# Performance work log

Measured on AMD Instinct MI355X. Metric: run time of the kernel, lower is better.

Reference implementation:

```python
import jax, jax.numpy as jnp
import numpy as np

EMBED = 1024
HEADS = 16
DH = EMBED // HEADS
B, S = 2, 2048


def setup_inputs() -> dict:
    key = jax.random.key(0)
    ks = jax.random.split(key, 12)
    inp = {
        "k": jax.random.normal(ks[0], (B, S, EMBED), jnp.float32),
        "q": jax.random.normal(ks[1], (B, S, EMBED), jnp.float32),
        "v": jax.random.normal(ks[2], (B, S, EMBED), jnp.float32),
        "mask": jax.random.randint(ks[3], (B, 1, S, S), 0, 2, jnp.int32),
        # per-head projections (shared across heads, as in the torch module)
        "Wk": jax.random.normal(ks[4], (DH, DH), jnp.float32) / np.sqrt(DH),
        "bk": jnp.zeros((DH,), jnp.float32),
        "Wq": jax.random.normal(ks[5], (DH, DH), jnp.float32) / np.sqrt(DH),
        "bq": jnp.zeros((DH,), jnp.float32),
        "Wv": jax.random.normal(ks[6], (DH, DH), jnp.float32) / np.sqrt(DH),
        "bv": jnp.zeros((DH,), jnp.float32),
        "Wo": jax.random.normal(ks[7], (EMBED, EMBED), jnp.float32) / np.sqrt(EMBED),
        "bo": jnp.zeros((EMBED,), jnp.float32),
    }
    return inp


def reference(k, q, v, mask, Wk, bk, Wq, bq, Wv, bv, Wo, bo):
    b, s, _ = k.shape
    sq = q.shape[1]
    # [B,S,H,dh]
    kh = k.reshape(b, s, HEADS, DH)
    qh = q.reshape(b, sq, HEADS, DH)
    vh = v.reshape(b, s, HEADS, DH)
    # per-head linear (weight shared across heads): x @ W.T + b
    kh = kh @ Wk.T + bk
    qh = qh @ Wq.T + bq
    vh = vh @ Wv.T + bv
    # scores [B,H,Sq,Sk]
    product = jnp.einsum("bqhd,bkhd->bhqk", qh, kh)
    # masked_fill BEFORE scaling, as in the original
    product = jnp.where(mask == 0, jnp.float32(-1e20), product)
    product = product / np.sqrt(DH)
    scores = jax.nn.softmax(product, axis=-1)
    ctx = jnp.einsum("bhqk,bkhd->bqhd", scores, vh).reshape(b, sq, EMBED)
    return ctx @ Wo.T + bo
```

## Files before the change

### kernel.cpp

```cpp
#include <hip/hip_runtime.h>
#include <hip/hip_bf16.h>
#include <math.h>

#define EMBED 1024
#define HEADS 16
#define DH    64
#define BATCH 2
#define SEQ   2048

typedef __attribute__((ext_vector_type(8))) short bf16x8;
typedef __attribute__((ext_vector_type(4))) short bf16x4;
typedef __attribute__((ext_vector_type(4))) float f32x4;
typedef unsigned long long u64;
typedef __attribute__((ext_vector_type(2))) unsigned long long u64x2;

#define QSCALE 0.1803368801111244f

static __device__ __forceinline__ unsigned short f2bf(float x) {
    unsigned u = __builtin_bit_cast(unsigned, x);
    return (unsigned short)((u + 0x7fffu + ((u >> 16) & 1u)) >> 16);
}
static __device__ __forceinline__ unsigned pk2bf(float a, float b) {
    union { __hip_bfloat162 h2; unsigned u; } c;
    c.h2 = __float22bfloat162_rn(make_float2(a, b));
    return c.u;
}
static __device__ __forceinline__ float fexp2(float x) {
#if __has_builtin(__builtin_amdgcn_exp2f)
    return __builtin_amdgcn_exp2f(x);
#else
    float r; asm("v_exp_f32 %0, %1" : "=v"(r) : "v"(x)); return r;
#endif
}
static __device__ __forceinline__ void gl_lds16(const void* g, void* l) {
    __builtin_amdgcn_global_load_lds(
        (const __attribute__((address_space(1))) void*)g,
        (__attribute__((address_space(3))) void*)l, 16, 0, 0);
}
static __device__ __forceinline__ bf16x8 cvt8(const float* p) {
    float4 a = ((const float4*)p)[0];
    float4 b = ((const float4*)p)[1];
    union { unsigned u[4]; bf16x8 v; } c;
    c.u[0] = pk2bf(a.x, a.y); c.u[1] = pk2bf(a.z, a.w);
    c.u[2] = pk2bf(b.x, b.y); c.u[3] = pk2bf(b.z, b.w);
    return c.v;
}

__global__ __launch_bounds__(256) void proj_mfma(
    const float* __restrict__ q, const float* __restrict__ k, const float* __restrict__ v,
    const float* __restrict__ Wq, const float* __restrict__ bq,
    const float* __restrict__ Wk, const float* __restrict__ bk,
    const float* __restrict__ Wv, const float* __restrict__ bv,
    unsigned short* __restrict__ qh, unsigned short* __restrict__ kh,
    unsigned short* __restrict__ vt,
    const int* __restrict__ mask, u64* __restrict__ bits,
    const float* __restrict__ Wo, unsigned short* __restrict__ Wob)
{
    const int blk   = blockIdx.x;
    const int which = blockIdx.y;
    const int t     = threadIdx.x;

    if (which == 3) {
        if (blk < 512) {
            const int idx = blk * 256 + t;
            const int4* src = (const int4*)(mask + (size_t)idx * 64);
            u64 wb = 0;
#pragma unroll
            for (int u = 0; u < 16; ++u) {
                int4 m = src[u];
                u64 nib = (m.x != 0 ? 1ull : 0) | (m.y != 0 ? 2ull : 0) |
                          (m.z != 0 ? 4ull : 0) | (m.w != 0 ? 8ull : 0);
                wb |= nib << (u * 4);
            }
            bits[idx] = wb;
        } else {
            const int i = ((blk - 512) * 256 + t) * 8;
            float4 a = ((const float4*)(Wo + i))[0];
            float4 b = ((const float4*)(Wo + i))[1];
            unsigned o32[4] = {pk2bf(a.x, a.y), pk2bf(a.z, a.w),
                               pk2bf(b.x, b.y), pk2bf(b.z, b.w)};
            *(uint4*)(Wob + i) = *(uint4*)o32;
        }
        return;
    }

    const float* x; const float* W; const float* bias;
    if (which == 0)      { x = q; W = Wq; bias = bq; }
    else if (which == 1) { x = k; W = Wk; bias = bk; }
    else                 { x = v; W = Wv; bias = bv; }

    __shared__ unsigned short Ws[64 * 72];

    const int w    = t >> 6;
    const int lane = t & 63;
    const int l15  = lane & 15;
    const int quad = lane >> 4;

    const int sr = t >> 2, sp = t & 3;
    {
        const float* wsrc = W + (size_t)sr * 64 + sp * 16;
        unsigned o32[8];
#pragma unroll
        for (int u4 = 0; u4 < 4; ++u4) {
            float4 a = ((const float4*)wsrc)[u4];
            o32[u4 * 2 + 0] = pk2bf(a.x, a.y);
            o32[u4 * 2 + 1] = pk2bf(a.z, a.w);
        }
        *(uint4*)&Ws[sr * 72 + sp * 16]     = *(uint4*)&o32[0];
        *(uint4*)&Ws[sr * 72 + sp * 16 + 8] = *(uint4*)&o32[4];
    }

    if (which == 2) {
        const int bh = blk >> 5;
        const int st = blk & 31;
        const int b  = bh >> 4, h = bh & 15;
        const int s  = st * 64 + w * 16 + l15;

        const float* xrow = x + ((size_t)(b * SEQ + s)) * EMBED + h * DH;
        const bf16x8 bx0 = cvt8(xrow + quad * 8);
        const bf16x8 bx1 = cvt8(xrow + 32 + quad * 8);

        __syncthreads();

#pragma unroll
        for (int nt = 0; nt < 4; ++nt) {
            bf16x8 aw0 = *(const bf16x8*)&Ws[(nt * 16 + l15) * 72 + quad * 8];
            bf16x8 aw1 = *(const bf16x8*)&Ws[(nt * 16 + l15) * 72 + 32 + quad * 8];
            f32x4 a = {0, 0, 0, 0};
            a = __builtin_amdgcn_mfma_f32_16x16x32_bf16(aw0, bx0, a, 0, 0, 0);
            a = __builtin_amdgcn_mfma_f32_16x16x32_bf16(aw1, bx1, a, 0, 0, 0);
#pragma unroll
            for (int r = 0; r < 4; ++r) {
                const int d = nt * 16 + quad * 4 + r;
                vt[((size_t)bh * DH + d) * SEQ + s] = f2bf(a[r] + bias[d]);
            }
        }
        return;
    }

    const float oscale = (which == 0) ? QSCALE : 1.0f;
    unsigned short* out = (which == 0) ? qh : kh;

    const float* xrow = x + ((size_t)blk * 64 + w * 16 + l15) * 64;
    const bf16x8 bx0 = cvt8(xrow + quad * 8);
    const bf16x8 bx1 = cvt8(xrow + 32 + quad * 8);

    __syncthreads();

    const int bs = blk * 4 + w;
    const int b = bs >> 11, s = bs & 2047;
    unsigned short* obase = out + (((size_t)b * HEADS + l15) * SEQ + s) * DH + quad * 4;

#pragma unroll
    for (int nt = 0; nt < 4; ++nt) {
        bf16x8 aw0 = *(const bf16x8*)&Ws[(nt * 16 + l15) * 72 + quad * 8];
        bf16x8 aw1 = *(const bf16x8*)&Ws[(nt * 16 + l15) * 72 + 32 + quad * 8];
        f32x4 a = {0, 0, 0, 0};
        a = __builtin_amdgcn_mfma_f32_16x16x32_bf16(aw0, bx0, a, 0, 0, 0);
        a = __builtin_amdgcn_mfma_f32_16x16x32_bf16(aw1, bx1, a, 0, 0, 0);
        const int d0 = nt * 16 + quad * 4;
        const float4 bb = *(const float4*)&bias[d0];
        unsigned o2[2] = {pk2bf((a[0] + bb.x) * oscale, (a[1] + bb.y) * oscale),
                          pk2bf((a[2] + bb.z) * oscale, (a[3] + bb.w) * oscale)};
        *(uint2*)(obase + nt * 16) = *(uint2*)o2;
    }
}

__global__ __launch_bounds__(256, 2) void attn_kernel(
    const unsigned short* __restrict__ qh, const unsigned short* __restrict__ kh,
    const unsigned short* __restrict__ vt, const u64* __restrict__ mbits,
    unsigned short* __restrict__ ctx)
{
    const int bid = blockIdx.x;
    const int bh  = bid & 31;
    const int q0  = (bid >> 5) * 128;
    const int b   = bh >> 4;

    __shared__ unsigned char smem[65536];

    const int t    = threadIdx.x;
    const int w    = t >> 6;
    const int lane = t & 63;
    const int l15  = lane & 15;
    const int quad = lane >> 4;

    const int srow   = lane >> 3;
    const int schunk = (lane & 7) ^ srow;

    bf16x8 qf[2][2];
#pragma unroll
    for (int g = 0; g < 2; ++g) {
        const unsigned short* qb =
            qh + ((size_t)bh * SEQ + q0 + w * 32 + g * 16 + l15) * DH + quad * 8;
        qf[g][0] = *(const bf16x8*)qb;
        qf[g][1] = *(const bf16x8*)(qb + 32);
    }

    f32x4 O[2][4];
#pragma unroll
    for (int g = 0; g < 2; ++g)
#pragma unroll
        for (int dt = 0; dt < 4; ++dt) O[g][dt] = f32x4{0, 0, 0, 0};
    f32x4 Osum[2] = {f32x4{0, 0, 0, 0}, f32x4{0, 0, 0, 0}};
    const bf16x4 ones = {(short)0x3F80, (short)0x3F80, (short)0x3F80, (short)0x3F80};

    const unsigned short* kbase = kh + (size_t)bh * SEQ * DH
                                  + (size_t)srow * DH + schunk * 8;
    const unsigned short* vbase = vt + (size_t)bh * DH * SEQ
                                  + (size_t)srow * SEQ + schunk * 8;
    const u64* mrow0 = mbits + ((size_t)b * SEQ + q0 + w * 32 + l15) * (SEQ / 64);
    const u64* mrow1 = mrow0 + 16 * (SEQ / 64);

    auto stage = [&](int kp, unsigned char* buf) {
#pragma unroll
        for (int j = 0; j < 8; ++j) {
            const int idx = w * 8 + j;
            if (idx < 16) {
                const int u = idx >> 3, i = idx & 7;
                gl_lds16(kbase + ((size_t)kp * 128 + u * 64 + i * 8) * DH,
                         buf + u * 8192 + i * 1024);
            } else {
                const int u = (idx - 16) >> 3, i = (idx - 16) & 7;
                gl_lds16(vbase + kp * 128 + u * 64 + (size_t)i * 8 * SEQ,
                         buf + 16384 + u * 8192 + i * 1024);
            }
        }
    };

    stage(0, smem);
    u64 pm00 = mrow0[0], pm01 = mrow0[1], pm10 = mrow1[0], pm11 = mrow1[1];
    __syncthreads();

    for (int it = 0; it < 16; ++it) {
        u64x2 nA, nB;
        if (it < 15) {
            nA = *(const u64x2*)&mrow0[2 * it + 2];
            nB = *(const u64x2*)&mrow1[2 * it + 2];
            stage(it + 1, smem + ((it + 1) & 1) * 32768);
            asm volatile("s_waitcnt vmcnt(10)" ::: "memory");
        } else {
            asm volatile("s_waitcnt vmcnt(0)" ::: "memory");
        }
        __builtin_amdgcn_s_barrier();
        __builtin_amdgcn_sched_barrier(0);

        const unsigned char* buf = smem + (it & 1) * 32768;

        __builtin_amdgcn_s_setprio(1);
#pragma unroll
        for (int u = 0; u < 2; ++u) {
            const unsigned short* KtH = (const unsigned short*)(buf + u * 8192);
            const unsigned short* VtH = (const unsigned short*)(buf + 16384 + u * 8192);
            const u64 mq0 = (u ? pm01 : pm00) >> (quad * 4);
            const u64 mq1 = (u ? pm11 : pm10) >> (quad * 4);

            bf16x4 p[2][4];
            const int rx = l15 & 7;
#pragma unroll
            for (int st = 0; st < 4; ++st) {
                const int r = st * 16 + l15;
                bf16x8 kf0 = *(const bf16x8*)&KtH[r * 64 + ((quad ^ rx)) * 8];
                bf16x8 kf1 = *(const bf16x8*)&KtH[r * 64 + ((quad ^ rx) ^ 4) * 8];
#pragma unroll
                for (int g = 0; g < 2; ++g) {
                    f32x4 sa = {0, 0, 0, 0};
                    sa = __builtin_amdgcn_mfma_f32_16x16x32_bf16(kf0, qf[g][0], sa, 0, 0, 0);
                    sa = __builtin_amdgcn_mfma_f32_16x16x32_bf16(kf1, qf[g][1], sa, 0, 0, 0);
                    const unsigned nib =
                        (unsigned)((g ? mq1 : mq0) >> (st * 16)) & 0xFu;
                    float p0 = (nib & 1u) ? fexp2(sa[0]) : 0.f;
                    float p1 = (nib & 2u) ? fexp2(sa[1]) : 0.f;
                    float p2 = (nib & 4u) ? fexp2(sa[2]) : 0.f;
                    float p3 = (nib & 8u) ? fexp2(sa[3]) : 0.f;
                    union { unsigned u2[2]; bf16x4 v; } pu;
                    pu.u2[0] = pk2bf(p0, p1);
                    pu.u2[1] = pk2bf(p2, p3);
                    p[g][st] = pu.v;
                    Osum[g] = __builtin_amdgcn_mfma_f32_16x16x16bf16_1k(
                        p[g][st], ones, Osum[g], 0, 0, 0);
                }
            }

#pragma unroll
            for (int dt = 0; dt < 4; ++dt) {
                const int d = dt * 16 + l15;
                const int dx = l15 & 7;
#pragma unroll
                for (int st = 0; st < 4; ++st) {
                    const int ch = (st * 2 + (quad >> 1)) ^ dx;
                    bf16x4 vb = *(const bf16x4*)&VtH[d * 64 + ch * 8 + (quad & 1) * 4];
                    O[0][dt] = __builtin_amdgcn_mfma_f32_16x16x16bf16_1k(
                        p[0][st], vb, O[0][dt], 0, 0, 0);
                    O[1][dt] = __builtin_amdgcn_mfma_f32_16x16x16bf16_1k(
                        p[1][st], vb, O[1][dt], 0, 0, 0);
                }
            }
        }
        __builtin_amdgcn_s_setprio(0);
        __builtin_amdgcn_sched_barrier(0);
        __builtin_amdgcn_s_barrier();

        if (it < 15) { pm00 = nA[0]; pm01 = nA[1]; pm10 = nB[0]; pm11 = nB[1]; }
    }

#pragma unroll
    for (int g = 0; g < 2; ++g) {
        float inv[4];
#pragma unroll
        for (int r = 0; r < 4; ++r) inv[r] = 1.0f / Osum[g][r];
#pragma unroll
        for (int r = 0; r < 4; ++r) {
            const int row = q0 + w * 32 + g * 16 + quad * 4 + r;
            unsigned short* dst = ctx + ((size_t)bh * SEQ + row) * DH + l15;
#pragma unroll
            for (int dt = 0; dt < 4; ++dt)
                dst[dt * 16] = f2bf(O[g][dt][r] * inv[r]);
        }
    }
}

__global__ __launch_bounds__(256, 3) void outproj_mfma(
    const unsigned short* __restrict__ ctx, const unsigned short* __restrict__ Wob,
    const float* __restrict__ bo, float* __restrict__ out)
{
    const int n0 = blockIdx.x * 64;
    const int m0 = blockIdx.y * 128;
    const int b  = m0 / SEQ;
    const int s0 = m0 % SEQ;

    __shared__ unsigned char smem[49152];

    const int t    = threadIdx.x;
    const int w    = t >> 6;
    const int lane = t & 63;
    const int l15  = lane & 15;
    const int quad = lane >> 4;
    const int srow   = lane >> 3;
    const int schunk = (lane & 7) ^ srow;

    const unsigned short* abase = ctx + ((size_t)b * HEADS * SEQ + s0 + srow) * DH + schunk * 8;
    const unsigned short* wbase = Wob + (size_t)(n0 + srow) * EMBED + schunk * 8;

    f32x4 acc[8];
#pragma unroll
    for (int mt = 0; mt < 8; ++mt) acc[mt] = f32x4{0, 0, 0, 0};

    auto stage = [&](int kt, unsigned char* buf) {
#pragma unroll
        for (int j = 0; j < 6; ++j) {
            const int idx = w * 6 + j;
            if (idx < 16)
                gl_lds16(abase + (size_t)kt * SEQ * DH + (size_t)idx * 8 * DH,
                         buf + idx * 1024);
            else
                gl_lds16(wbase + (size_t)(idx - 16) * 8 * EMBED + kt * 64,
                         buf + 16384 + (idx - 16) * 1024);
        }
    };

    stage(0, smem);
    __syncthreads();

    for (int kt = 0; kt < 16; ++kt) {
        if (kt < 15) stage(kt + 1, smem + ((kt + 1) & 1) * 24576);

        const unsigned char* buf = smem + (kt & 1) * 24576;
        const unsigned short* At = (const unsigned short*)buf;
        const unsigned short* Wt = (const unsigned short*)(buf + 16384);
        const int rx = l15 & 7;
        const int c0 = ((quad ^ rx)) * 8;

        __builtin_amdgcn_s_setprio(1);
        bf16x8 bf0 = *(const bf16x8*)&Wt[(w * 16 + l15) * 64 + c0];
        bf16x8 bf1 = *(const bf16x8*)&Wt[(w * 16 + l15) * 64 + (c0 ^ 32)];
#pragma unroll
        for (int mt = 0; mt < 8; ++mt) {
            bf16x8 af0 = *(const bf16x8*)&At[(mt * 16 + l15) * 64 + c0];
            bf16x8 af1 = *(const bf16x8*)&At[(mt * 16 + l15) * 64 + (c0 ^ 32)];
            acc[mt] = __builtin_amdgcn_mfma_f32_16x16x32_bf16(af0, bf0, acc[mt], 0, 0, 0);
            acc[mt] = __builtin_amdgcn_mfma_f32_16x16x32_bf16(af1, bf1, acc[mt], 0, 0, 0);
        }
        __builtin_amdgcn_s_setprio(0);
        __syncthreads();
    }

    const float bv = bo[n0 + w * 16 + l15];
#pragma unroll
    for (int mt = 0; mt < 8; ++mt) {
#pragma unroll
        for (int r = 0; r < 4; ++r) {
            out[(size_t)(m0 + mt * 16 + quad * 4 + r) * EMBED + n0 + w * 16 + l15] =
                acc[mt][r] + bv;
        }
    }
}

extern "C" void kernel_launch(void* const* d_in, const int* in_sizes, int n_in,
                              void* d_out, int out_size, void* d_ws, size_t ws_size,
                              hipStream_t stream) {
    const float* k    = (const float*)d_in[0];
    const float* q    = (const float*)d_in[1];
    const float* v    = (const float*)d_in[2];
    const int*   mask = (const int*)  d_in[3];
    const float* Wk   = (const float*)d_in[4];
    const float* bk   = (const float*)d_in[5];
    const float* Wq   = (const float*)d_in[6];
    const float* bq   = (const float*)d_in[7];
    const float* Wv   = (const float*)d_in[8];
    const float* bv   = (const float*)d_in[9];
    const float* Wo   = (const float*)d_in[10];
    const float* bo   = (const float*)d_in[11];
    float* out = (float*)d_out;

    const size_t TEN = (size_t)BATCH * HEADS * SEQ * DH;
    unsigned short* qh_bf = (unsigned short*)d_ws;
    unsigned short* kh_bf = qh_bf + TEN;
    unsigned short* vt_bf = kh_bf + TEN;
    unsigned short* ctxb  = vt_bf + TEN;
    unsigned short* Wob   = ctxb + TEN;
    u64*            mbits = (u64*)(Wob + EMBED * EMBED);

    proj_mfma<<<dim3(1024, 4), 256, 0, stream>>>(
        q, k, v, Wq, bq, Wk, bk, Wv, bv,
        qh_bf, kh_bf, vt_bf, mask, mbits, Wo, Wob);
    attn_kernel<<<dim3((SEQ / 128) * BATCH * HEADS), 256, 0, stream>>>(
        qh_bf, kh_bf, vt_bf, mbits, ctxb);
    outproj_mfma<<<dim3(EMBED / 64, BATCH * SEQ / 128), 256, 0, stream>>>(
        ctxb, Wob, bo, out);
}
```

Measured before the change: 217.0 us.

## Use 16x16x32 MFMA for PV product by permuting V^T columns

Stores V transposed with a permuted column order within each 64-key block, so that two adjacent 16x16x16 P tiles can be packed into a single bf16x8 operand. The PV and row-sum products then use the 16x16x32 MFMA, which halves the MFMA instruction count and replaces the 8-byte LDS reads of V with 16-byte reads. The next tile's K/V staging is also issued before the mask loads. The risk is that the permutation must match the k-index layout of the larger MFMA exactly, or the results are wrong.

```diff
diff --git a/kernel.cpp b/kernel.cpp
--- a/kernel.cpp
+++ b/kernel.cpp
@@ -114,7 +114,9 @@
         const int bh = blk >> 5;
         const int st = blk & 31;
         const int b  = bh >> 4, h = bh & 15;
-        const int s  = st * 64 + w * 16 + l15;
+        const int c  = w * 16 + l15;
+        const int s  = st * 64 + c;
+        const int cp = (c & 32) + ((c & 12) << 1) + ((c & 16) >> 2) + (c & 3);
 
         const float* xrow = x + ((size_t)(b * SEQ + s)) * EMBED + h * DH;
         const bf16x8 bx0 = cvt8(xrow + quad * 8);
@@ -132,7 +134,7 @@
 #pragma unroll
             for (int r = 0; r < 4; ++r) {
                 const int d = nt * 16 + quad * 4 + r;
-                vt[((size_t)bh * DH + d) * SEQ + s] = f2bf(a[r] + bias[d]);
+                vt[((size_t)bh * DH + d) * SEQ + st * 64 + cp] = f2bf(a[r] + bias[d]);
             }
         }
         return;
@@ -202,7 +204,8 @@
 #pragma unroll
         for (int dt = 0; dt < 4; ++dt) O[g][dt] = f32x4{0, 0, 0, 0};
     f32x4 Osum[2] = {f32x4{0, 0, 0, 0}, f32x4{0, 0, 0, 0}};
-    const bf16x4 ones = {(short)0x3F80, (short)0x3F80, (short)0x3F80, (short)0x3F80};
+    const bf16x8 ones8 = {(short)0x3F80, (short)0x3F80, (short)0x3F80, (short)0x3F80,
+                          (short)0x3F80, (short)0x3F80, (short)0x3F80, (short)0x3F80};
 
     const unsigned short* kbase = kh + (size_t)bh * SEQ * DH
                                   + (size_t)srow * DH + schunk * 8;
@@ -234,9 +237,9 @@
     for (int it = 0; it < 16; ++it) {
         u64x2 nA, nB;
         if (it < 15) {
+            stage(it + 1, smem + ((it + 1) & 1) * 32768);
             nA = *(const u64x2*)&mrow0[2 * it + 2];
             nB = *(const u64x2*)&mrow1[2 * it + 2];
-            stage(it + 1, smem + ((it + 1) & 1) * 32768);
             asm volatile("s_waitcnt vmcnt(10)" ::: "memory");
         } else {
             asm volatile("s_waitcnt vmcnt(0)" ::: "memory");
@@ -254,7 +257,7 @@
             const u64 mq0 = (u ? pm01 : pm00) >> (quad * 4);
             const u64 mq1 = (u ? pm11 : pm10) >> (quad * 4);
 
-            bf16x4 p[2][4];
+            unsigned pw[2][2][4];
             const int rx = l15 & 7;
 #pragma unroll
             for (int st = 0; st < 4; ++st) {
@@ -272,27 +275,35 @@
                     float p1 = (nib & 2u) ? fexp2(sa[1]) : 0.f;
                     float p2 = (nib & 4u) ? fexp2(sa[2]) : 0.f;
                     float p3 = (nib & 8u) ? fexp2(sa[3]) : 0.f;
-                    union { unsigned u2[2]; bf16x4 v; } pu;
-                    pu.u2[0] = pk2bf(p0, p1);
-                    pu.u2[1] = pk2bf(p2, p3);
-                    p[g][st] = pu.v;
-                    Osum[g] = __builtin_amdgcn_mfma_f32_16x16x16bf16_1k(
-                        p[g][st], ones, Osum[g], 0, 0, 0);
+                    pw[g][st >> 1][2 * (st & 1)]     = pk2bf(p0, p1);
+                    pw[g][st >> 1][2 * (st & 1) + 1] = pk2bf(p2, p3);
                 }
             }
+            bf16x8 p8[2][2];
+#pragma unroll
+            for (int g = 0; g < 2; ++g)
+#pragma unroll
+                for (int sp = 0; sp < 2; ++sp) {
+                    union { unsigned u4[4]; bf16x8 v; } pu;
+                    pu.u4[0] = pw[g][sp][0]; pu.u4[1] = pw[g][sp][1];
+                    pu.u4[2] = pw[g][sp][2]; pu.u4[3] = pw[g][sp][3];
+                    p8[g][sp] = pu.v;
+                    Osum[g] = __builtin_amdgcn_mfma_f32_16x16x32_bf16(
+                        p8[g][sp], ones8, Osum[g], 0, 0, 0);
+                }
 
 #pragma unroll
             for (int dt = 0; dt < 4; ++dt) {
                 const int d = dt * 16 + l15;
                 const int dx = l15 & 7;
 #pragma unroll
-                for (int st = 0; st < 4; ++st) {
-                    const int ch = (st * 2 + (quad >> 1)) ^ dx;
-                    bf16x4 vb = *(const bf16x4*)&VtH[d * 64 + ch * 8 + (quad & 1) * 4];
-                    O[0][dt] = __builtin_amdgcn_mfma_f32_16x16x16bf16_1k(
-                        p[0][st], vb, O[0][dt], 0, 0, 0);
-                    O[1][dt] = __builtin_amdgcn_mfma_f32_16x16x16bf16_1k(
-                        p[1][st], vb, O[1][dt], 0, 0, 0);
+                for (int sp = 0; sp < 2; ++sp) {
+                    const int ch = (sp * 4 + quad) ^ dx;
+                    bf16x8 vb = *(const bf16x8*)&VtH[d * 64 + ch * 8];
+                    O[0][dt] = __builtin_amdgcn_mfma_f32_16x16x32_bf16(
+                        p8[0][sp], vb, O[0][dt], 0, 0, 0);
+                    O[1][dt] = __builtin_amdgcn_mfma_f32_16x16x32_bf16(
+                        p8[1][sp], vb, O[1][dt], 0, 0, 0);
                 }
             }
         }
```

New measurement: 210.6 us (median of 2 runs). 2.9% less time.
